# Kernel optimization log

Hardware: AMD Instinct MI355X
Metric: run time of the kernel (lower is better)

## Reference

```python
import jax, jax.numpy as jnp
import numpy as np

NUM_ITERS = 3
NUM_SLOTS = 8
D = 128
MLP_HIDDEN = 128
EPS = 1e-8
LN_EPS = 1e-5
B, N = 64, 4096


def _layer_norm(x, g, b):
    m = jnp.mean(x, axis=-1, keepdims=True)
    v = jnp.mean(jnp.square(x - m), axis=-1, keepdims=True)
    return (x - m) * jax.lax.rsqrt(v + LN_EPS) * g + b


def setup_inputs() -> dict:
    key = jax.random.key(0)
    ks = jax.random.split(key, 16)
    s = 1.0 / np.sqrt(D)
    inp = {
        "x": jax.random.normal(ks[0], (B, N, D), jnp.float32),
        "slots_init": jax.random.normal(ks[1], (B, NUM_SLOTS, D), jnp.float32),
        "Wq": jax.random.normal(ks[2], (D, D), jnp.float32) * s,
        "bq": jnp.zeros((D,), jnp.float32),
        "Wk": jax.random.normal(ks[3], (D, D), jnp.float32) * s,
        "bk": jnp.zeros((D,), jnp.float32),
        "Wv": jax.random.normal(ks[4], (D, D), jnp.float32) * s,
        "bv": jnp.zeros((D,), jnp.float32),
        "g_in": jnp.ones((D,), jnp.float32), "b_in": jnp.zeros((D,), jnp.float32),
        "g_slot": jnp.ones((D,), jnp.float32), "b_slot": jnp.zeros((D,), jnp.float32),
        "g_mlp": jnp.ones((D,), jnp.float32), "b_mlp": jnp.zeros((D,), jnp.float32),
        "W1": jax.random.normal(ks[5], (MLP_HIDDEN, D), jnp.float32) * s,
        "b1": jnp.zeros((MLP_HIDDEN,), jnp.float32),
        "W2": jax.random.normal(ks[6], (D, MLP_HIDDEN), jnp.float32) * (1.0 / np.sqrt(MLP_HIDDEN)),
        "b2": jnp.zeros((D,), jnp.float32),
        "W_ih": jax.random.normal(ks[7], (3 * D, D), jnp.float32) * s,
        "W_hh": jax.random.normal(ks[8], (3 * D, D), jnp.float32) * s,
        "b_ih": jnp.zeros((3 * D,), jnp.float32),
        "b_hh": jnp.zeros((3 * D,), jnp.float32),
    }
    return inp


def _gru_cell(x, h, W_ih, W_hh, b_ih, b_hh):
    # torch.nn.GRUCell semantics
    gi = x @ W_ih.T + b_ih          # [.., 3D]
    gh = h @ W_hh.T + b_hh
    i_r, i_z, i_n = jnp.split(gi, 3, axis=-1)
    h_r, h_z, h_n = jnp.split(gh, 3, axis=-1)
    r = jax.nn.sigmoid(i_r + h_r)
    z = jax.nn.sigmoid(i_z + h_z)
    n = jnp.tanh(i_n + r * h_n)
    return (1.0 - z) * n + z * h


def reference(x, slots_init, Wq, bq, Wk, bk, Wv, bv, g_in, b_in, g_slot, b_slot,
              g_mlp, b_mlp, W1, b1, W2, b2, W_ih, W_hh, b_ih, b_hh):
    xn = _layer_norm(x, g_in, b_in)                 # [B,N,D]
    keys = xn @ Wk.T + bk                            # [B,N,D]
    values = xn @ Wv.T + bv                          # [B,N,D]
    scale = D ** -0.5
    slots = slots_init                               # [B,K,D]
    for _ in range(NUM_ITERS):
        prev = slots
        s = _layer_norm(slots, g_slot, b_slot)
        q = s @ Wq.T + bq                            # [B,K,D]
        logits = jnp.einsum('bid,bkd->bik', q, keys) * scale  # [B,K,N]
        attn = jax.nn.softmax(logits, axis=1)        # softmax over SLOT axis
        attn = attn + EPS
        attn = attn / jnp.sum(attn, axis=-1, keepdims=True)
        updates = jnp.einsum('bkd,bik->bid', values, attn)     # [B,K,D]
        slots = _gru_cell(updates.reshape(-1, D), prev.reshape(-1, D),
                          W_ih, W_hh, b_ih, b_hh).reshape(x.shape[0], -1, D)
        h = jax.nn.relu(_layer_norm(slots, g_mlp, b_mlp) @ W1.T + b1)
        slots = slots + (h @ W2.T + b2)
    return slots
```

## Files before the change

### kernel.cpp

```cpp
#include <hip/hip_runtime.h>
#include <hip/hip_bf16.h>

#define B_ 64
#define N_ 4096
#define KS 8
#define NCH 16
#define TP 136
#define LNEPS 1e-5f
#define EPSA 1e-8f
#define SCALE 0.08838834764831845f

typedef short short8  __attribute__((ext_vector_type(8)));
typedef short short4v __attribute__((ext_vector_type(4)));
typedef float f32x4   __attribute__((ext_vector_type(4)));

__device__ __forceinline__ unsigned short f2bf(float f) {
  union { float f; unsigned u; } v; v.f = f;
  unsigned r = v.u + 0x7fffu + ((v.u >> 16) & 1u);
  return (unsigned short)(r >> 16);
}
__device__ __forceinline__ float bflo(unsigned u) {
  union { unsigned u; float f; } c; c.u = u << 16; return c.f;
}
__device__ __forceinline__ float bfhi(unsigned u) {
  union { unsigned u; float f; } c; c.u = u & 0xffff0000u; return c.f;
}
__device__ __forceinline__ float sigmf(float x) { return 1.f / (1.f + __expf(-x)); }

__global__ __launch_bounds__(256) void prep_big(
    const float* __restrict__ Wih, const float* __restrict__ Whh,
    const float* __restrict__ Wq,  const float* __restrict__ Wk,
    const float* __restrict__ Wv,  const float* __restrict__ W1,
    const float* __restrict__ W2,
    const float* __restrict__ g_slot, const float* __restrict__ g_mlp,
    float* __restrict__ WgT, float* __restrict__ Mq,
    float* __restrict__ W1gT, float* __restrict__ W2T)
{
  int id = blockIdx.x * 256 + threadIdx.x;
  if (id < 49152) {
    int j = id >> 7, d = id & 127;
    float a = 0.f;
    for (int k = 0; k < 128; k++) a += Wih[j*128 + k] * Wv[k*128 + d];
    WgT[d*768 + j] = a;
  } else if (id < 65536) {
    int k = id - 49152; int d = k >> 7, t = k & 127;
    float a = 0.f;
    for (int j = 0; j < 128; j++) a += Wk[j*128 + t] * Wq[j*128 + d];
    Mq[d*128 + t] = a * SCALE * g_slot[d];
  } else if (id < 114688) {
    int k = id - 65536; int j = k >> 7, d = k & 127;
    WgT[d*768 + 384 + j] = Whh[j*128 + d];
  } else if (id < 131072) {
    int k = id - 114688; int t = k >> 7, d = k & 127;
    W1gT[d*128 + t] = W1[t*128 + d] * g_mlp[d];
  } else if (id < 147456) {
    int k = id - 131072; int t = k >> 7, d = k & 127;
    W2T[d*128 + t] = W2[t*128 + d];
  }
}

__global__ __launch_bounds__(256) void prep_small(
    const float* __restrict__ Wq, const float* __restrict__ Wk,
    const float* __restrict__ Wih, const float* __restrict__ W1,
    const float* __restrict__ bq, const float* __restrict__ bk,
    const float* __restrict__ bv, const float* __restrict__ b_ih,
    const float* __restrict__ b_hh, const float* __restrict__ b1,
    const float* __restrict__ b_mlp, const float* __restrict__ b_slot,
    const float* __restrict__ g_slot,
    float* __restrict__ cq_vec, float* __restrict__ wqcg,
    float* __restrict__ qc0g, float* __restrict__ bg, float* __restrict__ b1f)
{
  __shared__ float u[128], wqcr[128];
  int t = threadIdx.x;
  if (t < 128) {
    float a = bq[t];
    for (int d = 0; d < 128; d++) a += Wq[t*128 + d] * b_slot[d];
    u[t] = a;
  } else {
    int d = t - 128;
    float a = 0.f;
    for (int j = 0; j < 128; j++) a += Wq[j*128 + d] * bk[j];
    wqcr[d] = a * SCALE;
  }
  __syncthreads();
  if (t < 128) {
    float a = 0.f;
    for (int j = 0; j < 128; j++) a += Wk[j*128 + t] * u[j];
    cq_vec[t] = a * SCALE;
    wqcg[t] = wqcr[t] * g_slot[t];
  } else {
    int d = t - 128;
    float a = b1[d];
    for (int k = 0; k < 128; k++) a += W1[d*128 + k] * b_mlp[k];
    b1f[d] = a;
  }
  if (t < 64) {
    float v = wqcr[t]*b_slot[t] + wqcr[t+64]*b_slot[t+64]
            + SCALE*(bq[t]*bk[t] + bq[t+64]*bk[t+64]);
    #pragma unroll
    for (int st = 1; st < 64; st <<= 1) v += __shfl_xor(v, st);
    if (t == 0) *qc0g = v;
  }
  #pragma unroll
  for (int p = 0; p < 3; p++) {
    int j = t + p*256;
    if (j < 384) {
      float a = b_ih[j];
      for (int k = 0; k < 128; k++) a += Wih[j*128 + k] * bv[k];
      bg[j] = a;
    } else if (j < 768) {
      bg[j] = b_hh[j - 384];
    }
  }
}

__global__ __launch_bounds__(256) void ln_kernel(
    const float* __restrict__ x, const float* __restrict__ g_in, const float* __restrict__ b_in,
    unsigned short* __restrict__ xn)
{
  int tid = threadIdx.x;
  int rw = tid >> 2, cp = tid & 3;
  size_t row = (size_t)blockIdx.x * 64 + rw;
  const float* xrow = x + row * 128;
  float4 v[8];
  float s = 0.f, s2 = 0.f;
  #pragma unroll
  for (int i = 0; i < 8; i++) {
    v[i] = *(const float4*)(xrow + (cp + 4*i)*4);
    s  += v[i].x + v[i].y + v[i].z + v[i].w;
    s2 += v[i].x*v[i].x + v[i].y*v[i].y + v[i].z*v[i].z + v[i].w*v[i].w;
  }
  s += __shfl_xor(s, 1); s2 += __shfl_xor(s2, 1);
  s += __shfl_xor(s, 2); s2 += __shfl_xor(s2, 2);
  float mean = s * (1.f/128.f);
  float rstd = rsqrtf(s2 * (1.f/128.f) - mean*mean + LNEPS);
  #pragma unroll
  for (int i = 0; i < 8; i++) {
    int col = (cp + 4*i)*4;
    float4 gg = *(const float4*)(g_in + col);
    float4 bb = *(const float4*)(b_in + col);
    short4v pk;
    pk[0] = (short)f2bf((v[i].x - mean)*rstd*gg.x + bb.x);
    pk[1] = (short)f2bf((v[i].y - mean)*rstd*gg.y + bb.y);
    pk[2] = (short)f2bf((v[i].z - mean)*rstd*gg.z + bb.z);
    pk[3] = (short)f2bf((v[i].w - mean)*rstd*gg.w + bb.w);
    *(short4v*)(xn + row*128 + col) = pk;
  }
}

__global__ __launch_bounds__(64) void q_init_kernel(
    const float* __restrict__ slots_in, const float* __restrict__ Mq,
    const float* __restrict__ cq_vec, const float* __restrict__ wqcg,
    const float* __restrict__ qc0g,
    float* __restrict__ qt, float* __restrict__ qc)
{
  __shared__ float lnr[128];
  int row = blockIdx.x, t = threadIdx.x;
  float a = slots_in[row*128 + t], b = slots_in[row*128 + 64 + t];
  float s = a + b, s2 = a*a + b*b;
  #pragma unroll
  for (int st = 1; st < 64; st <<= 1) { s += __shfl_xor(s, st); s2 += __shfl_xor(s2, st); }
  float mean = s * (1.f/128.f);
  float rstd = rsqrtf(s2 * (1.f/128.f) - mean*mean + LNEPS);
  lnr[t] = (a - mean)*rstd; lnr[t+64] = (b - mean)*rstd;
  __syncthreads();
  float a0 = cq_vec[t], a1 = cq_vec[t+64];
  for (int d = 0; d < 128; d++) {
    float l = lnr[d];
    a0 += Mq[d*128 + t] * l;
    a1 += Mq[d*128 + 64 + t] * l;
  }
  qt[row*128 + t] = a0; qt[row*128 + 64 + t] = a1;
  float vq = wqcg[t]*lnr[t] + wqcg[t+64]*lnr[t+64];
  #pragma unroll
  for (int st = 1; st < 64; st <<= 1) vq += __shfl_xor(vq, st);
  if (t == 0) qc[row] = vq + *qc0g;
}

__global__ __launch_bounds__(256) void attn_kernel(
    const unsigned short* __restrict__ xn,
    const float* __restrict__ qt, const float* __restrict__ qc,
    float* __restrict__ Upart, float* __restrict__ Spart)
{
  __shared__ union ShMem {
    unsigned short xt[4][16][TP];
    float ured[4][8][128];
  } sh;
  __shared__ __align__(16) float pb[4][16][8];
  __shared__ float sred[4][8];

  const int tid = threadIdx.x;
  const int w = tid >> 6, lane = tid & 63;
  const int chunk = blockIdx.x, batch = blockIdx.y;
  const int m = lane & 15, quad = lane >> 4;

  short8 afrag[4];
  if (m < KS) {
    const float* qp = qt + (batch*KS + m)*128 + quad*8;
    #pragma unroll
    for (int kc = 0; kc < 4; kc++) {
      short8 a;
      #pragma unroll
      for (int j = 0; j < 8; j++) a[j] = (short)f2bf(qp[kc*32 + j]);
      afrag[kc] = a;
    }
  } else {
    #pragma unroll
    for (int kc = 0; kc < 4; kc++) {
      short8 a;
      #pragma unroll
      for (int j = 0; j < 8; j++) a[j] = 0;
      afrag[kc] = a;
    }
  }
  float creg[4];
  #pragma unroll
  for (int r = 0; r < 4; r++) creg[r] = qc[batch*KS + ((quad*4 + r) & 7)];

  float u0[8], u1[8], sac[4];
  #pragma unroll
  for (int i = 0; i < 8; i++) { u0[i] = 0.f; u1[i] = 0.f; }
  #pragma unroll
  for (int r = 0; r < 4; r++) sac[r] = 0.f;

  const unsigned short* xbase =
      xn + ((size_t)batch*N_ + chunk*256 + w*64 + m)*128 + quad*8;

  short8 cur[4], nxt[4];
  #pragma unroll
  for (int kc = 0; kc < 4; kc++) cur[kc] = *(const short8*)(xbase + kc*32);

  for (int g = 0; g < 4; g++) {
    if (g < 3) {
      #pragma unroll
      for (int kc = 0; kc < 4; kc++)
        nxt[kc] = *(const short8*)(xbase + (g+1)*2048 + kc*32);
    }
    #pragma unroll
    for (int kc = 0; kc < 4; kc++)
      *(short8*)&sh.xt[w][m][kc*32 + quad*8] = cur[kc];

    f32x4 acc = {0.f, 0.f, 0.f, 0.f};
    #pragma unroll
    for (int kc = 0; kc < 4; kc++)
      acc = __builtin_amdgcn_mfma_f32_16x16x32_bf16(afrag[kc], cur[kc], acc, 0, 0, 0);

    float l[4], o[4];
    #pragma unroll
    for (int r = 0; r < 4; r++) l[r] = acc[r] + creg[r];
    #pragma unroll
    for (int r = 0; r < 4; r++) o[r] = __shfl_xor(l[r], 16);
    float mx = fmaxf(fmaxf(fmaxf(l[0], l[1]), fmaxf(l[2], l[3])),
                     fmaxf(fmaxf(o[0], o[1]), fmaxf(o[2], o[3])));
    float e0 = __expf(l[0]-mx), e1 = __expf(l[1]-mx), e2 = __expf(l[2]-mx), e3 = __expf(l[3]-mx);
    float den = e0+e1+e2+e3 + __expf(o[0]-mx)+__expf(o[1]-mx)+__expf(o[2]-mx)+__expf(o[3]-mx);
    float rd = 1.f / den;
    float p0 = e0*rd + EPSA, p1 = e1*rd + EPSA, p2 = e2*rd + EPSA, p3 = e3*rd + EPSA;
    sac[0] += p0; sac[1] += p1; sac[2] += p2; sac[3] += p3;
    if (lane < 32) {
      float4 pv; pv.x = p0; pv.y = p1; pv.z = p2; pv.w = p3;
      *(float4*)&pb[w][m][quad*4] = pv;
    }

    #pragma unroll
    for (int t = 0; t < 16; t++) {
      float4 pA = *(const float4*)&pb[w][t][0];
      float4 pB = *(const float4*)&pb[w][t][4];
      unsigned vp = *(const unsigned*)&sh.xt[w][t][lane*2];
      float f0 = bflo(vp), f1 = bfhi(vp);
      u0[0] += pA.x*f0; u1[0] += pA.x*f1;
      u0[1] += pA.y*f0; u1[1] += pA.y*f1;
      u0[2] += pA.z*f0; u1[2] += pA.z*f1;
      u0[3] += pA.w*f0; u1[3] += pA.w*f1;
      u0[4] += pB.x*f0; u1[4] += pB.x*f1;
      u0[5] += pB.y*f0; u1[5] += pB.y*f1;
      u0[6] += pB.z*f0; u1[6] += pB.z*f1;
      u0[7] += pB.w*f0; u1[7] += pB.w*f1;
    }
    #pragma unroll
    for (int kc = 0; kc < 4; kc++) cur[kc] = nxt[kc];
  }

  #pragma unroll
  for (int st = 1; st < 16; st <<= 1) {
    #pragma unroll
    for (int r = 0; r < 4; r++) sac[r] += __shfl_xor(sac[r], st);
  }
  if (lane == 0)  { sred[w][0]=sac[0]; sred[w][1]=sac[1]; sred[w][2]=sac[2]; sred[w][3]=sac[3]; }
  if (lane == 16) { sred[w][4]=sac[0]; sred[w][5]=sac[1]; sred[w][6]=sac[2]; sred[w][7]=sac[3]; }

  __syncthreads();
  #pragma unroll
  for (int i = 0; i < 8; i++)
    *(float2*)&sh.ured[w][i][lane*2] = make_float2(u0[i], u1[i]);
  __syncthreads();

  {
    const float* ur = &sh.ured[0][0][0];
    int i4 = tid * 4;
    float4 a = *(const float4*)(ur + i4);
    float4 b = *(const float4*)(ur + 1024 + i4);
    float4 c = *(const float4*)(ur + 2048 + i4);
    float4 d = *(const float4*)(ur + 3072 + i4);
    float4 o4;
    o4.x = a.x+b.x+c.x+d.x; o4.y = a.y+b.y+c.y+d.y;
    o4.z = a.z+b.z+c.z+d.z; o4.w = a.w+b.w+c.w+d.w;
    *(float4*)(Upart + (size_t)(batch*NCH + chunk)*1024 + i4) = o4;
    if (tid < 8)
      Spart[(batch*NCH + chunk)*8 + tid] =
        sred[0][tid] + sred[1][tid] + sred[2][tid] + sred[3][tid];
  }
}

__global__ __launch_bounds__(256) void update_kernel(
    const float* __restrict__ slots_in, float* __restrict__ slots_out,
    const float* __restrict__ Upart, const float* __restrict__ Spart,
    const float* __restrict__ WgT, const float* __restrict__ bg,
    const float* __restrict__ W1gT, const float* __restrict__ b1f,
    const float* __restrict__ W2T, const float* __restrict__ b2,
    const float* __restrict__ Mq, const float* __restrict__ cq_vec,
    const float* __restrict__ wqcg, const float* __restrict__ qc0g,
    float* __restrict__ qt, float* __restrict__ qc)
{
  __shared__ float bu[128], hb[128], gg[768];
  __shared__ float s1[128], lnr[128], hmv[128], s2v[128], lnr2[128];
  __shared__ float stats[2], sSum;
  int row = blockIdx.x, t = threadIdx.x;
  int batch = row >> 3, slot = row & 7;

  float usum = 0.f;
  if (t < 128) {
    const float* Up = Upart + ((size_t)(batch*NCH)*8 + slot)*128 + t;
    #pragma unroll
    for (int c = 0; c < NCH; c++) usum += Up[(size_t)c*1024];
  } else {
    hb[t-128] = slots_in[row*128 + (t-128)];
    if (t < 192) {
      int l2 = t - 128;
      float sv = (l2 < NCH) ? Spart[(batch*NCH + l2)*8 + slot] : 0.f;
      #pragma unroll
      for (int st = 1; st < 16; st <<= 1) sv += __shfl_xor(sv, st);
      if (l2 == 0) sSum = sv;
    }
  }
  __syncthreads();
  if (t < 128) bu[t] = usum / sSum;
  __syncthreads();
  {
    float a0 = bg[t], a1 = bg[t+256], a2 = bg[t+512];
    const float* v1p = (t < 128) ? bu : hb;
    for (int d = 0; d < 128; d++) {
      float sd = bu[d], hd = hb[d], vd = v1p[d];
      const float* wr = WgT + d*768 + t;
      a0 += sd * wr[0];
      a1 += vd * wr[256];
      a2 += hd * wr[512];
    }
    gg[t] = a0; gg[t+256] = a1; gg[t+512] = a2;
  }
  __syncthreads();
  if (t < 128) {
    float r = sigmf(gg[t] + gg[384+t]);
    float z = sigmf(gg[128+t] + gg[512+t]);
    float n = tanhf(gg[256+t] + r * gg[640+t]);
    s1[t] = (1.f - z)*n + z*hb[t];
  }
  __syncthreads();
  if (t < 64) {
    float a = s1[t], b = s1[t+64];
    float s = a + b, s2 = a*a + b*b;
    #pragma unroll
    for (int st = 1; st < 64; st <<= 1) { s += __shfl_xor(s, st); s2 += __shfl_xor(s2, st); }
    if (t == 0) { float mean = s*(1.f/128.f); stats[0] = mean;
                  stats[1] = rsqrtf(s2*(1.f/128.f) - mean*mean + LNEPS); }
  }
  __syncthreads();
  if (t < 128) lnr[t] = (s1[t] - stats[0])*stats[1];
  __syncthreads();
  if (t < 128) {
    float a = b1f[t];
    for (int d = 0; d < 128; d++) a += W1gT[d*128 + t]*lnr[d];
    hmv[t] = fmaxf(a, 0.f);
  }
  __syncthreads();
  if (t < 128) {
    float a = s1[t] + b2[t];
    for (int d = 0; d < 128; d++) a += W2T[d*128 + t]*hmv[d];
    s2v[t] = a;
    slots_out[row*128 + t] = a;
  }
  __syncthreads();
  if (t < 64) {
    float a = s2v[t], b = s2v[t+64];
    float s = a + b, s2 = a*a + b*b;
    #pragma unroll
    for (int st = 1; st < 64; st <<= 1) { s += __shfl_xor(s, st); s2 += __shfl_xor(s2, st); }
    if (t == 0) { float mean = s*(1.f/128.f); stats[0] = mean;
                  stats[1] = rsqrtf(s2*(1.f/128.f) - mean*mean + LNEPS); }
  }
  __syncthreads();
  if (t < 128) lnr2[t] = (s2v[t] - stats[0])*stats[1];
  __syncthreads();
  if (t < 128) {
    float a = cq_vec[t];
    for (int d = 0; d < 128; d++) a += Mq[d*128 + t]*lnr2[d];
    qt[row*128 + t] = a;
  }
  if (t < 64) {
    float v = wqcg[t]*lnr2[t] + wqcg[t+64]*lnr2[t+64];
    #pragma unroll
    for (int st = 1; st < 64; st <<= 1) v += __shfl_xor(v, st);
    if (t == 0) qc[row] = v + *qc0g;
  }
}

extern "C" void kernel_launch(void* const* d_in, const int* in_sizes, int n_in,
                              void* d_out, int out_size, void* d_ws, size_t ws_size,
                              hipStream_t stream) {
  const float* x          = (const float*)d_in[0];
  const float* slots_init = (const float*)d_in[1];
  const float* Wq   = (const float*)d_in[2];
  const float* bq   = (const float*)d_in[3];
  const float* Wk   = (const float*)d_in[4];
  const float* bk   = (const float*)d_in[5];
  const float* Wv   = (const float*)d_in[6];
  const float* bv   = (const float*)d_in[7];
  const float* g_in = (const float*)d_in[8];
  const float* b_in = (const float*)d_in[9];
  const float* g_slot = (const float*)d_in[10];
  const float* b_slot = (const float*)d_in[11];
  const float* g_mlp  = (const float*)d_in[12];
  const float* b_mlp  = (const float*)d_in[13];
  const float* W1   = (const float*)d_in[14];
  const float* b1   = (const float*)d_in[15];
  const float* W2   = (const float*)d_in[16];
  const float* b2   = (const float*)d_in[17];
  const float* Wih  = (const float*)d_in[18];
  const float* Whh  = (const float*)d_in[19];
  const float* b_ih = (const float*)d_in[20];
  const float* b_hh = (const float*)d_in[21];

  char* p = (char*)d_ws;
  unsigned short* xn = (unsigned short*)p; p += (size_t)B_*N_*128*2;
  float* qt    = (float*)p; p += (size_t)B_*KS*128*4;
  float* qc    = (float*)p; p += (size_t)B_*KS*4 + 1024;
  float* slots = (float*)p; p += (size_t)B_*KS*128*4;
  float* Upart = (float*)p; p += (size_t)B_*NCH*KS*128*4;
  float* Spart = (float*)p; p += (size_t)B_*NCH*KS*4 + 1024;
  float* WgT   = (float*)p; p += 98304*4;
  float* Mq    = (float*)p; p += 16384*4;
  float* W1gT  = (float*)p; p += 16384*4;
  float* W2T   = (float*)p; p += 16384*4;
  float* cq_vec= (float*)p; p += 128*4;
  float* wqcg  = (float*)p; p += 128*4;
  float* qc0g  = (float*)p; p += 256;
  float* bg    = (float*)p; p += 768*4;
  float* b1f   = (float*)p; p += 128*4;

  ln_kernel<<<4096, 256, 0, stream>>>(x, g_in, b_in, xn);
  prep_big<<<576, 256, 0, stream>>>(Wih, Whh, Wq, Wk, Wv, W1, W2, g_slot, g_mlp,
                                    WgT, Mq, W1gT, W2T);
  prep_small<<<1, 256, 0, stream>>>(Wq, Wk, Wih, W1, bq, bk, bv, b_ih, b_hh, b1,
                                    b_mlp, b_slot, g_slot, cq_vec, wqcg, qc0g, bg, b1f);
  q_init_kernel<<<512, 64, 0, stream>>>(slots_init, Mq, cq_vec, wqcg, qc0g, qt, qc);

  attn_kernel<<<dim3(NCH, B_), 256, 0, stream>>>(xn, qt, qc, Upart, Spart);
  update_kernel<<<512, 256, 0, stream>>>(slots_init, slots, Upart, Spart,
      WgT, bg, W1gT, b1f, W2T, b2, Mq, cq_vec, wqcg, qc0g, qt, qc);

  attn_kernel<<<dim3(NCH, B_), 256, 0, stream>>>(xn, qt, qc, Upart, Spart);
  update_kernel<<<512, 256, 0, stream>>>(slots, slots, Upart, Spart,
      WgT, bg, W1gT, b1f, W2T, b2, Mq, cq_vec, wqcg, qc0g, qt, qc);

  attn_kernel<<<dim3(NCH, B_), 256, 0, stream>>>(xn, qt, qc, Upart, Spart);
  update_kernel<<<512, 256, 0, stream>>>(slots, (float*)d_out, Upart, Spart,
      WgT, bg, W1gT, b1f, W2T, b2, Mq, cq_vec, wqcg, qc0g, qt, qc);

  (void)in_sizes; (void)n_in; (void)out_size; (void)ws_size;
}
```

Before: 395.1 us.

## Fuse input layernorm into first attention pass and replace MFMA attention with FMA

The input layernorm is fused into a new first-iteration attention kernel, which normalizes x on the fly, writes the bf16 xn for later iterations and computes logits and updates in the same pass. This removes one full read of x and one read of xn. The attention kernels drop the MFMA and shared-memory transpose path in favor of per-lane FP32 FMA dot products with shuffle reductions, holding q fully in registers. The two prep kernels are merged into one launch. The price is much higher register pressure and scalar ALU work in place of matrix cores, and logits are now computed in fp32 rather than bf16.

After: 753.8 us. +90.8%, slower.

```diff
diff --git a/kernel.cpp b/kernel.cpp
--- a/kernel.cpp
+++ b/kernel.cpp
@@ -5,37 +5,83 @@
 #define N_ 4096
 #define KS 8
 #define NCH 16
-#define TP 136
 #define LNEPS 1e-5f
 #define EPSA 1e-8f
 #define SCALE 0.08838834764831845f
 
-typedef short short8  __attribute__((ext_vector_type(8)));
 typedef short short4v __attribute__((ext_vector_type(4)));
-typedef float f32x4   __attribute__((ext_vector_type(4)));
-
-__device__ __forceinline__ unsigned short f2bf(float f) {
-  union { float f; unsigned u; } v; v.f = f;
-  unsigned r = v.u + 0x7fffu + ((v.u >> 16) & 1u);
-  return (unsigned short)(r >> 16);
-}
+
 __device__ __forceinline__ float bflo(unsigned u) {
   union { unsigned u; float f; } c; c.u = u << 16; return c.f;
 }
 __device__ __forceinline__ float bfhi(unsigned u) {
   union { unsigned u; float f; } c; c.u = u & 0xffff0000u; return c.f;
 }
+__device__ __forceinline__ unsigned fbits(float f) {
+  union { float f; unsigned u; } c; c.f = f; return c.u;
+}
 __device__ __forceinline__ float sigmf(float x) { return 1.f / (1.f + __expf(-x)); }
 
-__global__ __launch_bounds__(256) void prep_big(
+__global__ __launch_bounds__(256) void prep_kernel(
     const float* __restrict__ Wih, const float* __restrict__ Whh,
     const float* __restrict__ Wq,  const float* __restrict__ Wk,
     const float* __restrict__ Wv,  const float* __restrict__ W1,
     const float* __restrict__ W2,
     const float* __restrict__ g_slot, const float* __restrict__ g_mlp,
+    const float* __restrict__ bq, const float* __restrict__ bk,
+    const float* __restrict__ bv, const float* __restrict__ b_ih,
+    const float* __restrict__ b_hh, const float* __restrict__ b1,
+    const float* __restrict__ b_mlp, const float* __restrict__ b_slot,
     float* __restrict__ WgT, float* __restrict__ Mq,
-    float* __restrict__ W1gT, float* __restrict__ W2T)
-{
+    float* __restrict__ W1gT, float* __restrict__ W2T,
+    float* __restrict__ cq_vec, float* __restrict__ wqcg,
+    float* __restrict__ qc0g, float* __restrict__ bg, float* __restrict__ b1f)
+{
+  if (blockIdx.x == 576) {
+    __shared__ float u[128], wqcr[128];
+    int t = threadIdx.x;
+    if (t < 128) {
+      float a = bq[t];
+      for (int d = 0; d < 128; d++) a += Wq[t*128 + d] * b_slot[d];
+      u[t] = a;
+    } else {
+      int d = t - 128;
+      float a = 0.f;
+      for (int j = 0; j < 128; j++) a += Wq[j*128 + d] * bk[j];
+      wqcr[d] = a * SCALE;
+    }
+    __syncthreads();
+    if (t < 128) {
+      float a = 0.f;
+      for (int j = 0; j < 128; j++) a += Wk[j*128 + t] * u[j];
+      cq_vec[t] = a * SCALE;
+      wqcg[t] = wqcr[t] * g_slot[t];
+    } else {
+      int d = t - 128;
+      float a = b1[d];
+      for (int k = 0; k < 128; k++) a += W1[d*128 + k] * b_mlp[k];
+      b1f[d] = a;
+    }
+    if (t < 64) {
+      float v = wqcr[t]*b_slot[t] + wqcr[t+64]*b_slot[t+64]
+              + SCALE*(bq[t]*bk[t] + bq[t+64]*bk[t+64]);
+      #pragma unroll
+      for (int st = 1; st < 64; st <<= 1) v += __shfl_xor(v, st);
+      if (t == 0) *qc0g = v;
+    }
+    #pragma unroll
+    for (int p = 0; p < 3; p++) {
+      int j = t + p*256;
+      if (j < 384) {
+        float a = b_ih[j];
+        for (int k = 0; k < 128; k++) a += Wih[j*128 + k] * bv[k];
+        bg[j] = a;
+      } else if (j < 768) {
+        bg[j] = b_hh[j - 384];
+      }
+    }
+    return;
+  }
   int id = blockIdx.x * 256 + threadIdx.x;
   if (id < 49152) {
     int j = id >> 7, d = id & 127;
@@ -59,95 +105,6 @@
   }
 }
 
-__global__ __launch_bounds__(256) void prep_small(
-    const float* __restrict__ Wq, const float* __restrict__ Wk,
-    const float* __restrict__ Wih, const float* __restrict__ W1,
-    const float* __restrict__ bq, const float* __restrict__ bk,
-    const float* __restrict__ bv, const float* __restrict__ b_ih,
-    const float* __restrict__ b_hh, const float* __restrict__ b1,
-    const float* __restrict__ b_mlp, const float* __restrict__ b_slot,
-    const float* __restrict__ g_slot,
-    float* __restrict__ cq_vec, float* __restrict__ wqcg,
-    float* __restrict__ qc0g, float* __restrict__ bg, float* __restrict__ b1f)
-{
-  __shared__ float u[128], wqcr[128];
-  int t = threadIdx.x;
-  if (t < 128) {
-    float a = bq[t];
-    for (int d = 0; d < 128; d++) a += Wq[t*128 + d] * b_slot[d];
-    u[t] = a;
-  } else {
-    int d = t - 128;
-    float a = 0.f;
-    for (int j = 0; j < 128; j++) a += Wq[j*128 + d] * bk[j];
-    wqcr[d] = a * SCALE;
-  }
-  __syncthreads();
-  if (t < 128) {
-    float a = 0.f;
-    for (int j = 0; j < 128; j++) a += Wk[j*128 + t] * u[j];
-    cq_vec[t] = a * SCALE;
-    wqcg[t] = wqcr[t] * g_slot[t];
-  } else {
-    int d = t - 128;
-    float a = b1[d];
-    for (int k = 0; k < 128; k++) a += W1[d*128 + k] * b_mlp[k];
-    b1f[d] = a;
-  }
-  if (t < 64) {
-    float v = wqcr[t]*b_slot[t] + wqcr[t+64]*b_slot[t+64]
-            + SCALE*(bq[t]*bk[t] + bq[t+64]*bk[t+64]);
-    #pragma unroll
-    for (int st = 1; st < 64; st <<= 1) v += __shfl_xor(v, st);
-    if (t == 0) *qc0g = v;
-  }
-  #pragma unroll
-  for (int p = 0; p < 3; p++) {
-    int j = t + p*256;
-    if (j < 384) {
-      float a = b_ih[j];
-      for (int k = 0; k < 128; k++) a += Wih[j*128 + k] * bv[k];
-      bg[j] = a;
-    } else if (j < 768) {
-      bg[j] = b_hh[j - 384];
-    }
-  }
-}
-
-__global__ __launch_bounds__(256) void ln_kernel(
-    const float* __restrict__ x, const float* __restrict__ g_in, const float* __restrict__ b_in,
-    unsigned short* __restrict__ xn)
-{
-  int tid = threadIdx.x;
-  int rw = tid >> 2, cp = tid & 3;
-  size_t row = (size_t)blockIdx.x * 64 + rw;
-  const float* xrow = x + row * 128;
-  float4 v[8];
-  float s = 0.f, s2 = 0.f;
-  #pragma unroll
-  for (int i = 0; i < 8; i++) {
-    v[i] = *(const float4*)(xrow + (cp + 4*i)*4);
-    s  += v[i].x + v[i].y + v[i].z + v[i].w;
-    s2 += v[i].x*v[i].x + v[i].y*v[i].y + v[i].z*v[i].z + v[i].w*v[i].w;
-  }
-  s += __shfl_xor(s, 1); s2 += __shfl_xor(s2, 1);
-  s += __shfl_xor(s, 2); s2 += __shfl_xor(s2, 2);
-  float mean = s * (1.f/128.f);
-  float rstd = rsqrtf(s2 * (1.f/128.f) - mean*mean + LNEPS);
-  #pragma unroll
-  for (int i = 0; i < 8; i++) {
-    int col = (cp + 4*i)*4;
-    float4 gg = *(const float4*)(g_in + col);
-    float4 bb = *(const float4*)(b_in + col);
-    short4v pk;
-    pk[0] = (short)f2bf((v[i].x - mean)*rstd*gg.x + bb.x);
-    pk[1] = (short)f2bf((v[i].y - mean)*rstd*gg.y + bb.y);
-    pk[2] = (short)f2bf((v[i].z - mean)*rstd*gg.z + bb.z);
-    pk[3] = (short)f2bf((v[i].w - mean)*rstd*gg.w + bb.w);
-    *(short4v*)(xn + row*128 + col) = pk;
-  }
-}
-
 __global__ __launch_bounds__(64) void q_init_kernel(
     const float* __restrict__ slots_in, const float* __restrict__ Mq,
     const float* __restrict__ cq_vec, const float* __restrict__ wqcg,
@@ -177,131 +134,88 @@
   if (t == 0) qc[row] = vq + *qc0g;
 }
 
-__global__ __launch_bounds__(256) void attn_kernel(
-    const unsigned short* __restrict__ xn,
+__device__ __forceinline__ void attn_token_step(
+    const float vf[8], const float qv[8][8], const float qcr[8],
+    float u[8][8], float* sacc)
+{
+  float lg[8];
+  #pragma unroll
+  for (int s8 = 0; s8 < 8; s8++) {
+    float p = qv[s8][0]*vf[0];
+    #pragma unroll
+    for (int j = 1; j < 8; j++) p += qv[s8][j]*vf[j];
+    p += __shfl_xor(p, 1);
+    p += __shfl_xor(p, 2);
+    p += __shfl_xor(p, 4);
+    p += __shfl_xor(p, 8);
+    lg[s8] = p + qcr[s8];
+  }
+  float mx = lg[0];
+  #pragma unroll
+  for (int s8 = 1; s8 < 8; s8++) mx = fmaxf(mx, lg[s8]);
+  float e[8], den = 0.f;
+  #pragma unroll
+  for (int s8 = 0; s8 < 8; s8++) { e[s8] = __expf(lg[s8]-mx); den += e[s8]; }
+  float rd = 1.f/den;
+  #pragma unroll
+  for (int s8 = 0; s8 < 8; s8++) {
+    float p = e[s8]*rd + EPSA;
+    sacc[s8] += p;
+    #pragma unroll
+    for (int j = 0; j < 8; j++) u[s8][j] += p*vf[j];
+  }
+}
+
+__device__ __forceinline__ void load_q(
     const float* __restrict__ qt, const float* __restrict__ qc,
+    int batch, int c, float qv[8][8], float qcr[8])
+{
+  #pragma unroll
+  for (int s8 = 0; s8 < 8; s8++) {
+    float4 qa = *(const float4*)(qt + (batch*KS + s8)*128 + c*8);
+    float4 qb = *(const float4*)(qt + (batch*KS + s8)*128 + c*8 + 4);
+    qv[s8][0]=qa.x; qv[s8][1]=qa.y; qv[s8][2]=qa.z; qv[s8][3]=qa.w;
+    qv[s8][4]=qb.x; qv[s8][5]=qb.y; qv[s8][6]=qb.z; qv[s8][7]=qb.w;
+    qcr[s8] = qc[batch*KS + s8];
+  }
+}
+
+__device__ __forceinline__ void attn_epilogue(
+    float u[8][8], float* sacc, float* uredf , float (*sred)[8],
+    int tid, int w, int lane, int chunk, int batch,
     float* __restrict__ Upart, float* __restrict__ Spart)
 {
-  __shared__ union ShMem {
-    unsigned short xt[4][16][TP];
-    float ured[4][8][128];
-  } sh;
-  __shared__ __align__(16) float pb[4][16][8];
-  __shared__ float sred[4][8];
-
-  const int tid = threadIdx.x;
-  const int w = tid >> 6, lane = tid & 63;
-  const int chunk = blockIdx.x, batch = blockIdx.y;
-  const int m = lane & 15, quad = lane >> 4;
-
-  short8 afrag[4];
-  if (m < KS) {
-    const float* qp = qt + (batch*KS + m)*128 + quad*8;
-    #pragma unroll
-    for (int kc = 0; kc < 4; kc++) {
-      short8 a;
-      #pragma unroll
-      for (int j = 0; j < 8; j++) a[j] = (short)f2bf(qp[kc*32 + j]);
-      afrag[kc] = a;
-    }
-  } else {
-    #pragma unroll
-    for (int kc = 0; kc < 4; kc++) {
-      short8 a;
-      #pragma unroll
-      for (int j = 0; j < 8; j++) a[j] = 0;
-      afrag[kc] = a;
-    }
-  }
-  float creg[4];
-  #pragma unroll
-  for (int r = 0; r < 4; r++) creg[r] = qc[batch*KS + ((quad*4 + r) & 7)];
-
-  float u0[8], u1[8], sac[4];
-  #pragma unroll
-  for (int i = 0; i < 8; i++) { u0[i] = 0.f; u1[i] = 0.f; }
-  #pragma unroll
-  for (int r = 0; r < 4; r++) sac[r] = 0.f;
-
-  const unsigned short* xbase =
-      xn + ((size_t)batch*N_ + chunk*256 + w*64 + m)*128 + quad*8;
-
-  short8 cur[4], nxt[4];
-  #pragma unroll
-  for (int kc = 0; kc < 4; kc++) cur[kc] = *(const short8*)(xbase + kc*32);
-
-  for (int g = 0; g < 4; g++) {
-    if (g < 3) {
-      #pragma unroll
-      for (int kc = 0; kc < 4; kc++)
-        nxt[kc] = *(const short8*)(xbase + (g+1)*2048 + kc*32);
-    }
-    #pragma unroll
-    for (int kc = 0; kc < 4; kc++)
-      *(short8*)&sh.xt[w][m][kc*32 + quad*8] = cur[kc];
-
-    f32x4 acc = {0.f, 0.f, 0.f, 0.f};
-    #pragma unroll
-    for (int kc = 0; kc < 4; kc++)
-      acc = __builtin_amdgcn_mfma_f32_16x16x32_bf16(afrag[kc], cur[kc], acc, 0, 0, 0);
-
-    float l[4], o[4];
-    #pragma unroll
-    for (int r = 0; r < 4; r++) l[r] = acc[r] + creg[r];
-    #pragma unroll
-    for (int r = 0; r < 4; r++) o[r] = __shfl_xor(l[r], 16);
-    float mx = fmaxf(fmaxf(fmaxf(l[0], l[1]), fmaxf(l[2], l[3])),
-                     fmaxf(fmaxf(o[0], o[1]), fmaxf(o[2], o[3])));
-    float e0 = __expf(l[0]-mx), e1 = __expf(l[1]-mx), e2 = __expf(l[2]-mx), e3 = __expf(l[3]-mx);
-    float den = e0+e1+e2+e3 + __expf(o[0]-mx)+__expf(o[1]-mx)+__expf(o[2]-mx)+__expf(o[3]-mx);
-    float rd = 1.f / den;
-    float p0 = e0*rd + EPSA, p1 = e1*rd + EPSA, p2 = e2*rd + EPSA, p3 = e3*rd + EPSA;
-    sac[0] += p0; sac[1] += p1; sac[2] += p2; sac[3] += p3;
-    if (lane < 32) {
-      float4 pv; pv.x = p0; pv.y = p1; pv.z = p2; pv.w = p3;
-      *(float4*)&pb[w][m][quad*4] = pv;
-    }
-
-    #pragma unroll
-    for (int t = 0; t < 16; t++) {
-      float4 pA = *(const float4*)&pb[w][t][0];
-      float4 pB = *(const float4*)&pb[w][t][4];
-      unsigned vp = *(const unsigned*)&sh.xt[w][t][lane*2];
-      float f0 = bflo(vp), f1 = bfhi(vp);
-      u0[0] += pA.x*f0; u1[0] += pA.x*f1;
-      u0[1] += pA.y*f0; u1[1] += pA.y*f1;
-      u0[2] += pA.z*f0; u1[2] += pA.z*f1;
-      u0[3] += pA.w*f0; u1[3] += pA.w*f1;
-      u0[4] += pB.x*f0; u1[4] += pB.x*f1;
-      u0[5] += pB.y*f0; u1[5] += pB.y*f1;
-      u0[6] += pB.z*f0; u1[6] += pB.z*f1;
-      u0[7] += pB.w*f0; u1[7] += pB.w*f1;
-    }
-    #pragma unroll
-    for (int kc = 0; kc < 4; kc++) cur[kc] = nxt[kc];
-  }
-
-  #pragma unroll
-  for (int st = 1; st < 16; st <<= 1) {
-    #pragma unroll
-    for (int r = 0; r < 4; r++) sac[r] += __shfl_xor(sac[r], st);
-  }
-  if (lane == 0)  { sred[w][0]=sac[0]; sred[w][1]=sac[1]; sred[w][2]=sac[2]; sred[w][3]=sac[3]; }
-  if (lane == 16) { sred[w][4]=sac[0]; sred[w][5]=sac[1]; sred[w][6]=sac[2]; sred[w][7]=sac[3]; }
-
-  __syncthreads();
-  #pragma unroll
-  for (int i = 0; i < 8; i++)
-    *(float2*)&sh.ured[w][i][lane*2] = make_float2(u0[i], u1[i]);
-  __syncthreads();
-
+  #pragma unroll
+  for (int s8 = 0; s8 < 8; s8++) {
+    #pragma unroll
+    for (int j = 0; j < 8; j++) {
+      float v = u[s8][j];
+      v += __shfl_xor(v, 16);
+      v += __shfl_xor(v, 32);
+      u[s8][j] = v;
+    }
+    float sv = sacc[s8];
+    sv += __shfl_xor(sv, 16);
+    sv += __shfl_xor(sv, 32);
+    if (lane == 0) sred[w][s8] = sv;
+  }
+  if (lane < 16) {
+    float* uw = uredf + w*1024;
+    #pragma unroll
+    for (int s8 = 0; s8 < 8; s8++) {
+      float4 A; A.x=u[s8][0]; A.y=u[s8][1]; A.z=u[s8][2]; A.w=u[s8][3];
+      float4 Bv; Bv.x=u[s8][4]; Bv.y=u[s8][5]; Bv.z=u[s8][6]; Bv.w=u[s8][7];
+      *(float4*)&uw[s8*128 + lane*8]     = A;
+      *(float4*)&uw[s8*128 + lane*8 + 4] = Bv;
+    }
+  }
+  __syncthreads();
   {
-    const float* ur = &sh.ured[0][0][0];
     int i4 = tid * 4;
-    float4 a = *(const float4*)(ur + i4);
-    float4 b = *(const float4*)(ur + 1024 + i4);
-    float4 c = *(const float4*)(ur + 2048 + i4);
-    float4 d = *(const float4*)(ur + 3072 + i4);
+    float4 a = *(const float4*)(uredf + i4);
+    float4 b = *(const float4*)(uredf + 1024 + i4);
+    float4 c = *(const float4*)(uredf + 2048 + i4);
+    float4 d = *(const float4*)(uredf + 3072 + i4);
     float4 o4;
     o4.x = a.x+b.x+c.x+d.x; o4.y = a.y+b.y+c.y+d.y;
     o4.z = a.z+b.z+c.z+d.z; o4.w = a.w+b.w+c.w+d.w;
@@ -310,6 +224,123 @@
       Spart[(batch*NCH + chunk)*8 + tid] =
         sred[0][tid] + sred[1][tid] + sred[2][tid] + sred[3][tid];
   }
+}
+
+__global__ __launch_bounds__(256, 2) void attn_kernel(
+    const unsigned short* __restrict__ xn,
+    const float* __restrict__ qt, const float* __restrict__ qc,
+    float* __restrict__ Upart, float* __restrict__ Spart)
+{
+  __shared__ float ured[4096];
+  __shared__ float sred[4][8];
+  const int tid = threadIdx.x;
+  const int w = tid >> 6, lane = tid & 63;
+  const int c = lane & 15;
+  const int chunk = blockIdx.x, batch = blockIdx.y;
+
+  float qv[8][8], qcr[8];
+  load_q(qt, qc, batch, c, qv, qcr);
+
+  float u[8][8], sacc[8];
+  #pragma unroll
+  for (int s8 = 0; s8 < 8; s8++) {
+    sacc[s8] = 0.f;
+    #pragma unroll
+    for (int j = 0; j < 8; j++) u[s8][j] = 0.f;
+  }
+
+  const int4* xb = (const int4*)(xn + ((size_t)batch*N_ + chunk*256 + w*64)*128);
+  int4 buf[4];
+  #pragma unroll
+  for (int i = 0; i < 4; i++) buf[i] = xb[i*64 + lane];
+
+  #pragma unroll
+  for (int s = 0; s < 16; s++) {
+    int4 cur = buf[s & 3];
+    if (s < 12) buf[s & 3] = xb[(s+4)*64 + lane];
+    float vf[8];
+    unsigned d0 = (unsigned)cur.x, d1 = (unsigned)cur.y,
+             d2 = (unsigned)cur.z, d3 = (unsigned)cur.w;
+    vf[0] = bflo(d0); vf[1] = bfhi(d0);
+    vf[2] = bflo(d1); vf[3] = bfhi(d1);
+    vf[4] = bflo(d2); vf[5] = bfhi(d2);
+    vf[6] = bflo(d3); vf[7] = bfhi(d3);
+    attn_token_step(vf, qv, qcr, u, sacc);
+  }
+  attn_epilogue(u, sacc, ured, sred, tid, w, lane, chunk, batch, Upart, Spart);
+}
+
+__global__ __launch_bounds__(256, 2) void attn0_kernel(
+    const float* __restrict__ x, const float* __restrict__ g_in, const float* __restrict__ b_in,
+    unsigned short* __restrict__ xn,
+    const float* __restrict__ qt, const float* __restrict__ qc,
+    float* __restrict__ Upart, float* __restrict__ Spart)
+{
+  __shared__ float ured[4096];
+  __shared__ float sred[4][8];
+  const int tid = threadIdx.x;
+  const int w = tid >> 6, lane = tid & 63;
+  const int c = lane & 15, tg = lane >> 4;
+  const int chunk = blockIdx.x, batch = blockIdx.y;
+
+  float qv[8][8], qcr[8];
+  load_q(qt, qc, batch, c, qv, qcr);
+  float4 gA = *(const float4*)(g_in + c*8), gB = *(const float4*)(g_in + c*8 + 4);
+  float4 bA = *(const float4*)(b_in + c*8), bB = *(const float4*)(b_in + c*8 + 4);
+
+  float u[8][8], sacc[8];
+  #pragma unroll
+  for (int s8 = 0; s8 < 8; s8++) {
+    sacc[s8] = 0.f;
+    #pragma unroll
+    for (int j = 0; j < 8; j++) u[s8][j] = 0.f;
+  }
+
+  const size_t tok0 = (size_t)batch*N_ + chunk*256 + w*64;
+  const float* xg0 = x + (tok0 + tg)*128 + c*8;
+  unsigned short* xnw = xn + (tok0 + tg)*128 + c*8;
+
+  float4 bufa[2], bufb[2];
+  #pragma unroll
+  for (int i = 0; i < 2; i++) {
+    bufa[i] = *(const float4*)(xg0 + i*512);
+    bufb[i] = *(const float4*)(xg0 + i*512 + 4);
+  }
+
+  #pragma unroll
+  for (int s = 0; s < 16; s++) {
+    float4 va = bufa[s & 1], vb = bufb[s & 1];
+    if (s < 14) {
+      bufa[s & 1] = *(const float4*)(xg0 + (s+2)*512);
+      bufb[s & 1] = *(const float4*)(xg0 + (s+2)*512 + 4);
+    }
+    float sm  = va.x + va.y + va.z + va.w + vb.x + vb.y + vb.z + vb.w;
+    float sq  = va.x*va.x + va.y*va.y + va.z*va.z + va.w*va.w
+              + vb.x*vb.x + vb.y*vb.y + vb.z*vb.z + vb.w*vb.w;
+    sm += __shfl_xor(sm, 1); sq += __shfl_xor(sq, 1);
+    sm += __shfl_xor(sm, 2); sq += __shfl_xor(sq, 2);
+    sm += __shfl_xor(sm, 4); sq += __shfl_xor(sq, 4);
+    sm += __shfl_xor(sm, 8); sq += __shfl_xor(sq, 8);
+    float mean = sm * (1.f/128.f);
+    float rstd = rsqrtf(sq * (1.f/128.f) - mean*mean + LNEPS);
+    float nf[8];
+    nf[0] = (va.x - mean)*rstd*gA.x + bA.x;
+    nf[1] = (va.y - mean)*rstd*gA.y + bA.y;
+    nf[2] = (va.z - mean)*rstd*gA.z + bA.z;
+    nf[3] = (va.w - mean)*rstd*gA.w + bA.w;
+    nf[4] = (vb.x - mean)*rstd*gB.x + bB.x;
+    nf[5] = (vb.y - mean)*rstd*gB.y + bB.y;
+    nf[6] = (vb.z - mean)*rstd*gB.z + bB.z;
+    nf[7] = (vb.w - mean)*rstd*gB.w + bB.w;
+    int4 st;
+    st.x = (int)__builtin_amdgcn_perm(fbits(nf[1]), fbits(nf[0]), 0x07060302u);
+    st.y = (int)__builtin_amdgcn_perm(fbits(nf[3]), fbits(nf[2]), 0x07060302u);
+    st.z = (int)__builtin_amdgcn_perm(fbits(nf[5]), fbits(nf[4]), 0x07060302u);
+    st.w = (int)__builtin_amdgcn_perm(fbits(nf[7]), fbits(nf[6]), 0x07060302u);
+    *(int4*)(xnw + s*512) = st;
+    attn_token_step(nf, qv, qcr, u, sacc);
+  }
+  attn_epilogue(u, sacc, ured, sred, tid, w, lane, chunk, batch, Upart, Spart);
 }
 
 __global__ __launch_bounds__(256) void update_kernel(
@@ -457,14 +488,12 @@
   float* bg    = (float*)p; p += 768*4;
   float* b1f   = (float*)p; p += 128*4;
 
-  ln_kernel<<<4096, 256, 0, stream>>>(x, g_in, b_in, xn);
-  prep_big<<<576, 256, 0, stream>>>(Wih, Whh, Wq, Wk, Wv, W1, W2, g_slot, g_mlp,
-                                    WgT, Mq, W1gT, W2T);
-  prep_small<<<1, 256, 0, stream>>>(Wq, Wk, Wih, W1, bq, bk, bv, b_ih, b_hh, b1,
-                                    b_mlp, b_slot, g_slot, cq_vec, wqcg, qc0g, bg, b1f);
+  prep_kernel<<<577, 256, 0, stream>>>(Wih, Whh, Wq, Wk, Wv, W1, W2, g_slot, g_mlp,
+                                       bq, bk, bv, b_ih, b_hh, b1, b_mlp, b_slot,
+                                       WgT, Mq, W1gT, W2T, cq_vec, wqcg, qc0g, bg, b1f);
   q_init_kernel<<<512, 64, 0, stream>>>(slots_init, Mq, cq_vec, wqcg, qc0g, qt, qc);
 
-  attn_kernel<<<dim3(NCH, B_), 256, 0, stream>>>(xn, qt, qc, Upart, Spart);
+  attn0_kernel<<<dim3(NCH, B_), 256, 0, stream>>>(x, g_in, b_in, xn, qt, qc, Upart, Spart);
   update_kernel<<<512, 256, 0, stream>>>(slots_init, slots, Upart, Spart,
       WgT, bg, W1gT, b1f, W2T, b2, Mq, cq_vec, wqcg, qc0g, qt, qc);
 
```
